# Kernel optimization log

Measured on AMD Instinct MI355X. Metric: run time of the kernel, lower is better.

## Reference

```python
import jax, jax.numpy as jnp
import numpy as np

TEMPERATURE = 0.07
EPS = 1e-12  # F.normalize eps


def _l2norm(x):
    n = jnp.linalg.norm(x, axis=-1, keepdims=True)
    return x / jnp.maximum(n, EPS)


def setup_inputs() -> dict:
    key = jax.random.key(0)
    k1, k2 = jax.random.split(key)
    B, T, H = 16, 512, 1024
    h_source = jax.random.normal(k1, (B, T, H), dtype=jnp.float32)
    h_target = jax.random.normal(k2, (B, T, H), dtype=jnp.float32)
    src_mask = jnp.ones((B, T), dtype=bool)
    tgt_mask = jnp.ones((B, T), dtype=bool)
    return {"h_source": h_source, "h_target": h_target,
            "src_mask": src_mask, "tgt_mask": tgt_mask}


def reference(h_source, h_target, src_mask, tgt_mask):
    # Masks are all-True and B*T == max_samples, so boolean selection == reshape
    # and the random subsampling branch is never taken (deterministic path).
    H = h_source.shape[-1]
    h_s = h_source.reshape(-1, H).astype(jnp.float32)          # (N, H)
    h_t = jax.lax.stop_gradient(h_target.reshape(-1, H)).astype(jnp.float32)  # detached

    h_s_norm = _l2norm(h_s)                                     # (N, H)
    h_t_norm = _l2norm(h_t)                                     # (M, H)
    sim = h_s_norm @ h_t_norm.T                                 # (N, M) cosine sim

    pos_idx = jnp.argmax(sim, axis=1)                           # == topk_idx[:, 0]
    logits = sim / TEMPERATURE
    # cross-entropy with pos_idx labels (stable log-softmax)
    logp = jax.nn.log_softmax(logits, axis=1)
    l_contrastive = -jnp.mean(jnp.take_along_axis(logp, pos_idx[:, None], axis=1)[:, 0])

    # contextual consistency: adjacent source tokens' NN embeddings should align
    nn_embeds = h_t_norm[pos_idx]                               # (N, H)
    nn_sim = jnp.sum(nn_embeds[:-1] * nn_embeds[1:], axis=-1)   # (N-1,)
    l_contextual = 1.0 - jnp.mean(nn_sim)

    return (l_contrastive, l_contextual)
```

## Files before the change

kernel.cpp:

```cpp
#include <hip/hip_runtime.h>
#include <hip/hip_bf16.h>
#include <stdint.h>


#define HDIM 1024
#define NROW 8192
#define TEMP_INV (1.0f / 0.07f)

typedef __attribute__((ext_vector_type(4))) float float4v;
typedef __attribute__((ext_vector_type(2))) float float2v;

#define SN_OFF   ((size_t)0)
#define TN_OFF   ((size_t)8388608)
#define POS_OFF  ((size_t)16777216)
#define SUM_OFF  (POS_OFF + 32768)
#define PMX_OFF  (SUM_OFF + 32768)
#define ACC_OFF  (PMX_OFF + 65536)

static __device__ __forceinline__ void gload_lds16(const void* gptr, void* lptr) {
    __builtin_amdgcn_global_load_lds(
        (const __attribute__((address_space(1))) void*)gptr,
        (__attribute__((address_space(3))) void*)(uintptr_t)(uint32_t)(uintptr_t)lptr,
        16, 0, 0);
}

static __device__ __forceinline__ float fp8dot4(unsigned a, unsigned b) {
    float2v al = __builtin_amdgcn_cvt_pk_f32_fp8((int)a, false);
    float2v ah = __builtin_amdgcn_cvt_pk_f32_fp8((int)a, true);
    float2v bl = __builtin_amdgcn_cvt_pk_f32_fp8((int)b, false);
    float2v bh = __builtin_amdgcn_cvt_pk_f32_fp8((int)b, true);
    return al[0]*bl[0] + al[1]*bl[1] + ah[0]*bh[0] + ah[1]*bh[1];
}

__global__ __launch_bounds__(256)
void norm_kernel(const float* __restrict__ hs, const float* __restrict__ ht,
                 char* __restrict__ Sn, char* __restrict__ Tn,
                 float* __restrict__ sumexp, unsigned long long* __restrict__ pmax,
                 float* __restrict__ acc) {
    const int b = blockIdx.x;
    const int t = threadIdx.x;
    const int r = t >> 4, c = t & 15;
    const float* in;
    char* outg;
    if (b < 512) { in = hs + (size_t)(b * 16 + r) * HDIM;        outg = Sn + (size_t)b * 16384; }
    else         { in = ht + (size_t)((b - 512) * 16 + r) * HDIM; outg = Tn + (size_t)(b - 512) * 16384; }

    float4v v[16];
    float ss = 0.f;
    #pragma unroll
    for (int i = 0; i < 16; ++i) {
        v[i] = ((const float4v*)in)[c * 16 + i];
        ss += v[i][0]*v[i][0] + v[i][1]*v[i][1] + v[i][2]*v[i][2] + v[i][3]*v[i][3];
    }
    #pragma unroll
    for (int off = 1; off < 16; off <<= 1) ss += __shfl_xor(ss, off);
    const float sc = 1.0f / fmaxf(sqrtf(ss), 1e-12f);

    #pragma unroll
    for (int h = 0; h < 2; ++h) {
        #pragma unroll
        for (int q = 0; q < 4; ++q) {
            const int vi = h * 8 + q * 2;
            int d0 = __builtin_amdgcn_cvt_pk_fp8_f32(v[vi][0]*sc, v[vi][1]*sc, 0, false);
            d0     = __builtin_amdgcn_cvt_pk_fp8_f32(v[vi][2]*sc, v[vi][3]*sc, d0, true);
            int d1 = __builtin_amdgcn_cvt_pk_fp8_f32(v[vi+1][0]*sc, v[vi+1][1]*sc, 0, false);
            d1     = __builtin_amdgcn_cvt_pk_fp8_f32(v[vi+1][2]*sc, v[vi+1][3]*sc, d1, true);
            uint2 pk; pk.x = (unsigned)d0; pk.y = (unsigned)d1;
            *(uint2*)(outg + (c * 2 + h) * 512 + q * 128 + r * 8) = pk;
        }
    }

    if (b < 512 && t < 16) { sumexp[b * 16 + t] = 0.f; pmax[b * 16 + t] = 0ull; }
    if (b == 0 && t == 16) { acc[0] = 0.f; acc[1] = 0.f; }
}

__global__ __launch_bounds__(512, 4)
void flash_kernel(const char* __restrict__ Sn, const char* __restrict__ Tn,
                  float* __restrict__ sumexp, unsigned long long* __restrict__ pmax) {
    __shared__ __align__(16) char As[16384];
    __shared__ __align__(16) char Bs[8192];
    __shared__ float stSe[256];
    __shared__ unsigned long long stPk[256];
    const int t = threadIdx.x;
    const int wave = t >> 6, lane = t & 63;
    const int quad = lane >> 4, l16 = lane & 15;
    const int rbase  = (int)(blockIdx.x & 31) * 256;
    const int cbase0 = (int)(blockIdx.x >> 5) * 512;

    if (t < 256) { stSe[t] = 0.f; stPk[t] = 0ull; }

    const int wm = (wave & 3) * 64, wn = (wave >> 2) * 64;

    const char* gaBase0 = Sn + (size_t)(rbase / 16 + wave * 2 + 0) * 16384 + lane * 16;
    const char* gaBase1 = Sn + (size_t)(rbase / 16 + wave * 2 + 1) * 16384 + lane * 16;

    for (int s = 0; s < 4; ++s) {
        const int cbase = cbase0 + s * 128;
        const char* ga0 = gaBase0;
        const char* ga1 = gaBase1;
        const char* gb  = Tn + (size_t)(cbase / 16 + wave) * 16384 + lane * 16;

        float4v acc[4][4];
        #pragma unroll
        for (int i = 0; i < 4; ++i)
            #pragma unroll
            for (int j = 0; j < 4; ++j) acc[i][j] = (float4v){0.f, 0.f, 0.f, 0.f};

        for (int kb = 0; kb < 16; ++kb) {
            gload_lds16(ga0, As + (wave * 2 + 0) * 1024);
            gload_lds16(ga1, As + (wave * 2 + 1) * 1024);
            gload_lds16(gb,  Bs + wave * 1024);
            ga0 += 1024; ga1 += 1024; gb += 1024;
            __syncthreads();
            #pragma unroll
            for (int ks = 0; ks < 2; ++ks) {
                long af[4], bf[4];
                #pragma unroll
                for (int i = 0; i < 4; ++i)
                    af[i] = *(const long*)(As + ((wave & 3) * 4 + i) * 1024 + ks * 512 + lane * 8);
                #pragma unroll
                for (int j = 0; j < 4; ++j)
                    bf[j] = *(const long*)(Bs + ((wave >> 2) * 4 + j) * 1024 + ks * 512 + lane * 8);
                #pragma unroll
                for (int i = 0; i < 4; ++i)
                    #pragma unroll
                    for (int j = 0; j < 4; ++j)
                        acc[i][j] = __builtin_amdgcn_mfma_f32_16x16x32_fp8_fp8(af[i], bf[j], acc[i][j], 0, 0, 0);
            }
            __syncthreads();
        }

        float* pbSe = (float*)Bs;
        unsigned long long* pbPk = (unsigned long long*)(Bs + 1024);
        float se_v[4][4]; unsigned long long pk_v[4][4];
        #pragma unroll
        for (int i = 0; i < 4; ++i) {
            #pragma unroll
            for (int r = 0; r < 4; ++r) {
                float se = 0.f; float mx = -2.f; int mi = 0x7fffffff;
                #pragma unroll
                for (int j = 0; j < 4; ++j) {
                    float v = acc[i][j][r];
                    se += __expf(v * TEMP_INV);
                    int col = cbase + wn + j * 16 + l16;
                    if (v > mx || (v == mx && col < mi)) { mx = v; mi = col; }
                }
                #pragma unroll
                for (int off = 1; off < 16; off <<= 1) {
                    se += __shfl_xor(se, off);
                    float om = __shfl_xor(mx, off);
                    int oi = __shfl_xor(mi, off);
                    if (om > mx || (om == mx && oi < mi)) { mx = om; mi = oi; }
                }
                se_v[i][r] = se;
                pk_v[i][r] = ((unsigned long long)__float_as_uint(mx + 2.0f) << 32)
                             | (unsigned long long)(0xffffffffu - (unsigned)mi);
            }
        }
        if (wave < 4 && l16 == 0) {
            #pragma unroll
            for (int i = 0; i < 4; ++i)
                #pragma unroll
                for (int r = 0; r < 4; ++r) {
                    int rl = wm + i * 16 + quad * 4 + r;
                    pbSe[rl] = se_v[i][r]; pbPk[rl] = pk_v[i][r];
                }
        }
        __syncthreads();
        if (wave >= 4 && l16 == 0) {
            #pragma unroll
            for (int i = 0; i < 4; ++i)
                #pragma unroll
                for (int r = 0; r < 4; ++r) {
                    int rl = wm + i * 16 + quad * 4 + r;
                    float se = se_v[i][r] + pbSe[rl];
                    unsigned long long pk = pk_v[i][r];
                    unsigned long long po = pbPk[rl];
                    if (po > pk) pk = po;
                    stSe[rl] += se;
                    if (pk > stPk[rl]) stPk[rl] = pk;
                }
        }
        __syncthreads();
    }

    if (t < 256) {
        atomicAdd(&sumexp[rbase + t], stSe[t]);
        atomicMax(&pmax[rbase + t], stPk[t]);
    }
}

__global__ void rowloss_kernel(const float* __restrict__ sumexp,
                               const unsigned long long* __restrict__ pmax,
                               int* __restrict__ pos, float* __restrict__ acc) {
    int r = blockIdx.x * 256 + threadIdx.x;
    unsigned long long p = pmax[r];
    float mx = __uint_as_float((unsigned)(p >> 32)) - 2.0f;
    pos[r] = (int)(0xffffffffu - (unsigned)(p & 0xffffffffu));
    float loss = logf(sumexp[r]) - mx * TEMP_INV;
    #pragma unroll
    for (int off = 1; off < 64; off <<= 1) loss += __shfl_xor(loss, off);
    __shared__ float red[4];
    if ((threadIdx.x & 63) == 0) red[threadIdx.x >> 6] = loss;
    __syncthreads();
    if (threadIdx.x == 0) atomicAdd(acc + 0, red[0] + red[1] + red[2] + red[3]);
}

__global__ __launch_bounds__(256)
void ctx_kernel(const char* __restrict__ Tn,
                const int* __restrict__ pos, float* __restrict__ acc) {
    const int wave = threadIdx.x >> 6, lane = threadIdx.x & 63;
    const int wid = blockIdx.x * 4 + wave;
    float s = 0.f;
    for (int g = wid; g < NROW - 1; g += 1024) {
        int ia = pos[g], ib = pos[g + 1];
        #pragma unroll
        for (int h = 0; h < 2; ++h) {
            int p = lane + h * 64;
            int off = (p >> 2) * 512 + (p & 3) * 128;
            uint2 va = *(const uint2*)(Tn + (size_t)(ia >> 4) * 16384 + off + (ia & 15) * 8);
            uint2 vb = *(const uint2*)(Tn + (size_t)(ib >> 4) * 16384 + off + (ib & 15) * 8);
            s += fp8dot4(va.x, vb.x);
            s += fp8dot4(va.y, vb.y);
        }
    }
    #pragma unroll
    for (int off = 1; off < 64; off <<= 1) s += __shfl_xor(s, off);
    __shared__ float red[4];
    if (lane == 0) red[wave] = s;
    __syncthreads();
    if (threadIdx.x == 0) atomicAdd(acc + 1, red[0] + red[1] + red[2] + red[3]);
}

__global__ void fin_kernel(const float* __restrict__ acc, float* __restrict__ out) {
    out[0] = acc[0] / (float)NROW;
    out[1] = 1.0f - acc[1] / (float)(NROW - 1);
}

extern "C" void kernel_launch(void* const* d_in, const int* in_sizes, int n_in,
                              void* d_out, int out_size, void* d_ws, size_t ws_size,
                              hipStream_t stream) {
    const float* hs = (const float*)d_in[0];
    const float* ht = (const float*)d_in[1];
    char* ws = (char*)d_ws;
    char* Sn = ws + SN_OFF;
    char* Tn = ws + TN_OFF;
    int*   pos = (int*)(ws + POS_OFF);
    float* sumexp = (float*)(ws + SUM_OFF);
    unsigned long long* pmax = (unsigned long long*)(ws + PMX_OFF);
    float* acc = (float*)(ws + ACC_OFF);
    float* out = (float*)d_out;

    norm_kernel<<<1024, 256, 0, stream>>>(hs, ht, Sn, Tn, sumexp, pmax, acc);
    flash_kernel<<<512, 512, 0, stream>>>(Sn, Tn, sumexp, pmax);
    rowloss_kernel<<<NROW / 256, 256, 0, stream>>>(sumexp, pmax, pos, acc);
    ctx_kernel<<<256, 256, 0, stream>>>(Tn, pos, acc);
    fin_kernel<<<1, 1, 0, stream>>>(acc, out);
}
```

Before: 254.9 us.

## Widen flash block to 1024 threads with 256x256 tiles and add row-major target copy

```diff
diff --git a/kernel.cpp b/kernel.cpp
--- a/kernel.cpp
+++ b/kernel.cpp
@@ -12,7 +12,8 @@
 
 #define SN_OFF   ((size_t)0)
 #define TN_OFF   ((size_t)8388608)
-#define POS_OFF  ((size_t)16777216)
+#define TR_OFF   ((size_t)16777216)
+#define POS_OFF  ((size_t)25165824)
 #define SUM_OFF  (POS_OFF + 32768)
 #define PMX_OFF  (SUM_OFF + 32768)
 #define ACC_OFF  (PMX_OFF + 65536)
@@ -34,7 +35,7 @@
 
 __global__ __launch_bounds__(256)
 void norm_kernel(const float* __restrict__ hs, const float* __restrict__ ht,
-                 char* __restrict__ Sn, char* __restrict__ Tn,
+                 char* __restrict__ Sn, char* __restrict__ Tn, char* __restrict__ Tr,
                  float* __restrict__ sumexp, unsigned long long* __restrict__ pmax,
                  float* __restrict__ acc) {
     const int b = blockIdx.x;
@@ -42,8 +43,10 @@
     const int r = t >> 4, c = t & 15;
     const float* in;
     char* outg;
+    char* outr = nullptr;
     if (b < 512) { in = hs + (size_t)(b * 16 + r) * HDIM;        outg = Sn + (size_t)b * 16384; }
-    else         { in = ht + (size_t)((b - 512) * 16 + r) * HDIM; outg = Tn + (size_t)(b - 512) * 16384; }
+    else         { in = ht + (size_t)((b - 512) * 16 + r) * HDIM; outg = Tn + (size_t)(b - 512) * 16384;
+                   outr = Tr + (size_t)((b - 512) * 16 + r) * HDIM; }
 
     float4v v[16];
     float ss = 0.f;
@@ -67,6 +70,7 @@
             d1     = __builtin_amdgcn_cvt_pk_fp8_f32(v[vi+1][2]*sc, v[vi+1][3]*sc, d1, true);
             uint2 pk; pk.x = (unsigned)d0; pk.y = (unsigned)d1;
             *(uint2*)(outg + (c * 2 + h) * 512 + q * 128 + r * 8) = pk;
+            if (outr) *(uint2*)(outr + c * 64 + h * 32 + q * 8) = pk;
         }
     }
 
@@ -74,11 +78,11 @@
     if (b == 0 && t == 16) { acc[0] = 0.f; acc[1] = 0.f; }
 }
 
-__global__ __launch_bounds__(512, 4)
+__global__ __launch_bounds__(1024, 4)
 void flash_kernel(const char* __restrict__ Sn, const char* __restrict__ Tn,
                   float* __restrict__ sumexp, unsigned long long* __restrict__ pmax) {
     __shared__ __align__(16) char As[16384];
-    __shared__ __align__(16) char Bs[8192];
+    __shared__ __align__(16) char Bs[16384];
     __shared__ float stSe[256];
     __shared__ unsigned long long stPk[256];
     const int t = threadIdx.x;
@@ -90,15 +94,12 @@
     if (t < 256) { stSe[t] = 0.f; stPk[t] = 0ull; }
 
     const int wm = (wave & 3) * 64, wn = (wave >> 2) * 64;
-
-    const char* gaBase0 = Sn + (size_t)(rbase / 16 + wave * 2 + 0) * 16384 + lane * 16;
-    const char* gaBase1 = Sn + (size_t)(rbase / 16 + wave * 2 + 1) * 16384 + lane * 16;
-
-    for (int s = 0; s < 4; ++s) {
-        const int cbase = cbase0 + s * 128;
-        const char* ga0 = gaBase0;
-        const char* ga1 = gaBase1;
-        const char* gb  = Tn + (size_t)(cbase / 16 + wave) * 16384 + lane * 16;
+    const char* gaBase = Sn + (size_t)(rbase / 16 + wave) * 16384 + lane * 16;
+
+    for (int s = 0; s < 2; ++s) {
+        const int cbase = cbase0 + s * 256;
+        const char* ga = gaBase;
+        const char* gb = Tn + (size_t)(cbase / 16 + wave) * 16384 + lane * 16;
 
         float4v acc[4][4];
         #pragma unroll
@@ -107,10 +108,9 @@
             for (int j = 0; j < 4; ++j) acc[i][j] = (float4v){0.f, 0.f, 0.f, 0.f};
 
         for (int kb = 0; kb < 16; ++kb) {
-            gload_lds16(ga0, As + (wave * 2 + 0) * 1024);
-            gload_lds16(ga1, As + (wave * 2 + 1) * 1024);
-            gload_lds16(gb,  Bs + wave * 1024);
-            ga0 += 1024; ga1 += 1024; gb += 1024;
+            gload_lds16(ga, As + wave * 1024);
+            gload_lds16(gb, Bs + wave * 1024);
+            ga += 1024; gb += 1024;
             __syncthreads();
             #pragma unroll
             for (int ks = 0; ks < 2; ++ks) {
@@ -131,7 +131,7 @@
         }
 
         float* pbSe = (float*)Bs;
-        unsigned long long* pbPk = (unsigned long long*)(Bs + 1024);
+        unsigned long long* pbPk = (unsigned long long*)(Bs + 4096);
         float se_v[4][4]; unsigned long long pk_v[4][4];
         #pragma unroll
         for (int i = 0; i < 4; ++i) {
@@ -157,29 +157,28 @@
                              | (unsigned long long)(0xffffffffu - (unsigned)mi);
             }
         }
-        if (wave < 4 && l16 == 0) {
+        if (l16 == 0) {
+            const int wc = wave >> 2;
             #pragma unroll
             for (int i = 0; i < 4; ++i)
                 #pragma unroll
                 for (int r = 0; r < 4; ++r) {
                     int rl = wm + i * 16 + quad * 4 + r;
-                    pbSe[rl] = se_v[i][r]; pbPk[rl] = pk_v[i][r];
+                    pbSe[wc * 256 + rl] = se_v[i][r];
+                    pbPk[wc * 256 + rl] = pk_v[i][r];
                 }
         }
         __syncthreads();
-        if (wave >= 4 && l16 == 0) {
-            #pragma unroll
-            for (int i = 0; i < 4; ++i)
-                #pragma unroll
-                for (int r = 0; r < 4; ++r) {
-                    int rl = wm + i * 16 + quad * 4 + r;
-                    float se = se_v[i][r] + pbSe[rl];
-                    unsigned long long pk = pk_v[i][r];
-                    unsigned long long po = pbPk[rl];
-                    if (po > pk) pk = po;
-                    stSe[rl] += se;
-                    if (pk > stPk[rl]) stPk[rl] = pk;
-                }
+        if (t < 256) {
+            float se = 0.f; unsigned long long pk = 0ull;
+            #pragma unroll
+            for (int w = 0; w < 4; ++w) {
+                se += pbSe[w * 256 + t];
+                unsigned long long po = pbPk[w * 256 + t];
+                if (po > pk) pk = po;
+            }
+            stSe[t] += se;
+            if (pk > stPk[t]) stPk[t] = pk;
         }
         __syncthreads();
     }
@@ -207,22 +206,17 @@
 }
 
 __global__ __launch_bounds__(256)
-void ctx_kernel(const char* __restrict__ Tn,
+void ctx_kernel(const char* __restrict__ Tr,
                 const int* __restrict__ pos, float* __restrict__ acc) {
     const int wave = threadIdx.x >> 6, lane = threadIdx.x & 63;
     const int wid = blockIdx.x * 4 + wave;
     float s = 0.f;
     for (int g = wid; g < NROW - 1; g += 1024) {
         int ia = pos[g], ib = pos[g + 1];
-        #pragma unroll
-        for (int h = 0; h < 2; ++h) {
-            int p = lane + h * 64;
-            int off = (p >> 2) * 512 + (p & 3) * 128;
-            uint2 va = *(const uint2*)(Tn + (size_t)(ia >> 4) * 16384 + off + (ia & 15) * 8);
-            uint2 vb = *(const uint2*)(Tn + (size_t)(ib >> 4) * 16384 + off + (ib & 15) * 8);
-            s += fp8dot4(va.x, vb.x);
-            s += fp8dot4(va.y, vb.y);
-        }
+        uint4 va = ((const uint4*)(Tr + (size_t)ia * HDIM))[lane];
+        uint4 vb = ((const uint4*)(Tr + (size_t)ib * HDIM))[lane];
+        s += fp8dot4(va.x, vb.x) + fp8dot4(va.y, vb.y)
+           + fp8dot4(va.z, vb.z) + fp8dot4(va.w, vb.w);
     }
     #pragma unroll
     for (int off = 1; off < 64; off <<= 1) s += __shfl_xor(s, off);
@@ -245,15 +239,16 @@
     char* ws = (char*)d_ws;
     char* Sn = ws + SN_OFF;
     char* Tn = ws + TN_OFF;
+    char* Tr = ws + TR_OFF;
     int*   pos = (int*)(ws + POS_OFF);
     float* sumexp = (float*)(ws + SUM_OFF);
     unsigned long long* pmax = (unsigned long long*)(ws + PMX_OFF);
     float* acc = (float*)(ws + ACC_OFF);
     float* out = (float*)d_out;
 
-    norm_kernel<<<1024, 256, 0, stream>>>(hs, ht, Sn, Tn, sumexp, pmax, acc);
-    flash_kernel<<<512, 512, 0, stream>>>(Sn, Tn, sumexp, pmax);
+    norm_kernel<<<1024, 256, 0, stream>>>(hs, ht, Sn, Tn, Tr, sumexp, pmax, acc);
+    flash_kernel<<<512, 1024, 0, stream>>>(Sn, Tn, sumexp, pmax);
     rowloss_kernel<<<NROW / 256, 256, 0, stream>>>(sumexp, pmax, pos, acc);
-    ctx_kernel<<<256, 256, 0, stream>>>(Tn, pos, acc);
+    ctx_kernel<<<256, 256, 0, stream>>>(Tr, pos, acc);
     fin_kernel<<<1, 1, 0, stream>>>(acc, out);
 }
```

After: 270.4 us. +6.0%, slower.

## Fuse tail kernels and add row-major FP8 target copy with coalesced norm loads

Applied to the files above, without the earlier changes.

```diff
diff --git a/kernel.cpp b/kernel.cpp
--- a/kernel.cpp
+++ b/kernel.cpp
@@ -12,10 +12,11 @@
 
 #define SN_OFF   ((size_t)0)
 #define TN_OFF   ((size_t)8388608)
-#define POS_OFF  ((size_t)16777216)
-#define SUM_OFF  (POS_OFF + 32768)
+#define TR_OFF   ((size_t)16777216)
+#define SUM_OFF  ((size_t)25165824)
 #define PMX_OFF  (SUM_OFF + 32768)
 #define ACC_OFF  (PMX_OFF + 65536)
+#define CNT_OFF  (ACC_OFF + 64)
 
 static __device__ __forceinline__ void gload_lds16(const void* gptr, void* lptr) {
     __builtin_amdgcn_global_load_lds(
@@ -34,44 +35,54 @@
 
 __global__ __launch_bounds__(256)
 void norm_kernel(const float* __restrict__ hs, const float* __restrict__ ht,
-                 char* __restrict__ Sn, char* __restrict__ Tn,
+                 char* __restrict__ Sn, char* __restrict__ Tn, char* __restrict__ Tr,
                  float* __restrict__ sumexp, unsigned long long* __restrict__ pmax,
-                 float* __restrict__ acc) {
+                 float* __restrict__ acc, unsigned* __restrict__ cnt) {
     const int b = blockIdx.x;
     const int t = threadIdx.x;
-    const int r = t >> 4, c = t & 15;
-    const float* in;
-    char* outg;
-    if (b < 512) { in = hs + (size_t)(b * 16 + r) * HDIM;        outg = Sn + (size_t)b * 16384; }
-    else         { in = ht + (size_t)((b - 512) * 16 + r) * HDIM; outg = Tn + (size_t)(b - 512) * 16384; }
+    const int wave = t >> 6, lane = t & 63;
+    const bool isT = (b >= 512);
+    const int g = isT ? (b - 512) : b;
+    const float* in = (isT ? ht : hs) + (size_t)g * 16 * HDIM;
+    char* outTiled = (isT ? Tn : Sn) + (size_t)g * 16384;
+
+    __shared__ float sq[16][256];
+    __shared__ float sscale[16];
 
     float4v v[16];
-    float ss = 0.f;
     #pragma unroll
     for (int i = 0; i < 16; ++i) {
-        v[i] = ((const float4v*)in)[c * 16 + i];
-        ss += v[i][0]*v[i][0] + v[i][1]*v[i][1] + v[i][2]*v[i][2] + v[i][3]*v[i][3];
-    }
-    #pragma unroll
-    for (int off = 1; off < 16; off <<= 1) ss += __shfl_xor(ss, off);
-    const float sc = 1.0f / fmaxf(sqrtf(ss), 1e-12f);
-
-    #pragma unroll
-    for (int h = 0; h < 2; ++h) {
-        #pragma unroll
-        for (int q = 0; q < 4; ++q) {
-            const int vi = h * 8 + q * 2;
-            int d0 = __builtin_amdgcn_cvt_pk_fp8_f32(v[vi][0]*sc, v[vi][1]*sc, 0, false);
-            d0     = __builtin_amdgcn_cvt_pk_fp8_f32(v[vi][2]*sc, v[vi][3]*sc, d0, true);
-            int d1 = __builtin_amdgcn_cvt_pk_fp8_f32(v[vi+1][0]*sc, v[vi+1][1]*sc, 0, false);
-            d1     = __builtin_amdgcn_cvt_pk_fp8_f32(v[vi+1][2]*sc, v[vi+1][3]*sc, d1, true);
-            uint2 pk; pk.x = (unsigned)d0; pk.y = (unsigned)d1;
-            *(uint2*)(outg + (c * 2 + h) * 512 + q * 128 + r * 8) = pk;
-        }
-    }
-
-    if (b < 512 && t < 16) { sumexp[b * 16 + t] = 0.f; pmax[b * 16 + t] = 0ull; }
-    if (b == 0 && t == 16) { acc[0] = 0.f; acc[1] = 0.f; }
+        v[i] = ((const float4v*)in)[i * 256 + t];
+        sq[i][t] = v[i][0]*v[i][0] + v[i][1]*v[i][1] + v[i][2]*v[i][2] + v[i][3]*v[i][3];
+    }
+    __syncthreads();
+    #pragma unroll
+    for (int j = 0; j < 4; ++j) {
+        const int ri = wave * 4 + j;
+        float s = sq[ri][lane] + sq[ri][lane + 64] + sq[ri][lane + 128] + sq[ri][lane + 192];
+        #pragma unroll
+        for (int off = 1; off < 64; off <<= 1) s += __shfl_xor(s, off);
+        if (lane == 0) sscale[ri] = 1.0f / fmaxf(sqrtf(s), 1e-12f);
+    }
+    __syncthreads();
+
+    char* tiled = (char*)sq;
+    const int koff = (t >> 3) * 512 + ((t >> 1) & 3) * 128 + (t & 1) * 4;
+    #pragma unroll
+    for (int i = 0; i < 16; ++i) {
+        const float sc = sscale[i];
+        int d = __builtin_amdgcn_cvt_pk_fp8_f32(v[i][0]*sc, v[i][1]*sc, 0, false);
+        d     = __builtin_amdgcn_cvt_pk_fp8_f32(v[i][2]*sc, v[i][3]*sc, d, true);
+        *(int*)(tiled + koff + i * 8) = d;
+        if (isT) ((int*)(Tr + (size_t)(g * 16 + i) * HDIM))[t] = d;
+    }
+    __syncthreads();
+    #pragma unroll
+    for (int j = 0; j < 4; ++j)
+        ((uint4*)outTiled)[j * 256 + t] = ((const uint4*)tiled)[j * 256 + t];
+
+    if (!isT && t < 16) { sumexp[b * 16 + t] = 0.f; pmax[b * 16 + t] = 0ull; }
+    if (b == 0 && t == 16) { acc[0] = 0.f; acc[1] = 0.f; *cnt = 0u; }
 }
 
 __global__ __launch_bounds__(512, 4)
@@ -90,7 +101,6 @@
     if (t < 256) { stSe[t] = 0.f; stPk[t] = 0ull; }
 
     const int wm = (wave & 3) * 64, wn = (wave >> 2) * 64;
-
     const char* gaBase0 = Sn + (size_t)(rbase / 16 + wave * 2 + 0) * 16384 + lane * 16;
     const char* gaBase1 = Sn + (size_t)(rbase / 16 + wave * 2 + 1) * 16384 + lane * 16;
 
@@ -190,38 +200,37 @@
     }
 }
 
-__global__ void rowloss_kernel(const float* __restrict__ sumexp,
-                               const unsigned long long* __restrict__ pmax,
-                               int* __restrict__ pos, float* __restrict__ acc) {
-    int r = blockIdx.x * 256 + threadIdx.x;
-    unsigned long long p = pmax[r];
-    float mx = __uint_as_float((unsigned)(p >> 32)) - 2.0f;
-    pos[r] = (int)(0xffffffffu - (unsigned)(p & 0xffffffffu));
-    float loss = logf(sumexp[r]) - mx * TEMP_INV;
-    #pragma unroll
-    for (int off = 1; off < 64; off <<= 1) loss += __shfl_xor(loss, off);
-    __shared__ float red[4];
-    if ((threadIdx.x & 63) == 0) red[threadIdx.x >> 6] = loss;
-    __syncthreads();
-    if (threadIdx.x == 0) atomicAdd(acc + 0, red[0] + red[1] + red[2] + red[3]);
-}
-
 __global__ __launch_bounds__(256)
-void ctx_kernel(const char* __restrict__ Tn,
-                const int* __restrict__ pos, float* __restrict__ acc) {
-    const int wave = threadIdx.x >> 6, lane = threadIdx.x & 63;
-    const int wid = blockIdx.x * 4 + wave;
+void tail_kernel(const float* __restrict__ sumexp,
+                 const unsigned long long* __restrict__ pmax,
+                 const char* __restrict__ Tr,
+                 float* __restrict__ acc, unsigned* __restrict__ cnt,
+                 float* __restrict__ out) {
+    const int blk = blockIdx.x;
+    const int t = threadIdx.x, wave = t >> 6, lane = t & 63;
+
+    if (wave == 0) {
+        int r = blk * 32 + (lane & 31);
+        unsigned long long p = pmax[r];
+        float mx = __uint_as_float((unsigned)(p >> 32)) - 2.0f;
+        float loss = logf(sumexp[r]) - mx * TEMP_INV;
+        #pragma unroll
+        for (int off = 1; off < 32; off <<= 1) loss += __shfl_xor(loss, off);
+        if (lane == 0) atomicAdd(acc + 0, loss);
+    }
+
     float s = 0.f;
-    for (int g = wid; g < NROW - 1; g += 1024) {
-        int ia = pos[g], ib = pos[g + 1];
-        #pragma unroll
-        for (int h = 0; h < 2; ++h) {
-            int p = lane + h * 64;
-            int off = (p >> 2) * 512 + (p & 3) * 128;
-            uint2 va = *(const uint2*)(Tn + (size_t)(ia >> 4) * 16384 + off + (ia & 15) * 8);
-            uint2 vb = *(const uint2*)(Tn + (size_t)(ib >> 4) * 16384 + off + (ib & 15) * 8);
-            s += fp8dot4(va.x, vb.x);
-            s += fp8dot4(va.y, vb.y);
+    #pragma unroll
+    for (int it = 0; it < 8; ++it) {
+        int g = blk * 32 + wave * 8 + it;
+        if (g < NROW - 1) {
+            unsigned long long pa = pmax[g], pb = pmax[g + 1];
+            int ia = (int)(0xffffffffu - (unsigned)(pa & 0xffffffffu));
+            int ib = (int)(0xffffffffu - (unsigned)(pb & 0xffffffffu));
+            uint4 va = ((const uint4*)(Tr + (size_t)ia * HDIM))[lane];
+            uint4 vb = ((const uint4*)(Tr + (size_t)ib * HDIM))[lane];
+            s += fp8dot4(va.x, vb.x) + fp8dot4(va.y, vb.y)
+               + fp8dot4(va.z, vb.z) + fp8dot4(va.w, vb.w);
         }
     }
     #pragma unroll
@@ -229,12 +238,18 @@
     __shared__ float red[4];
     if (lane == 0) red[wave] = s;
     __syncthreads();
-    if (threadIdx.x == 0) atomicAdd(acc + 1, red[0] + red[1] + red[2] + red[3]);
-}
-
-__global__ void fin_kernel(const float* __restrict__ acc, float* __restrict__ out) {
-    out[0] = acc[0] / (float)NROW;
-    out[1] = 1.0f - acc[1] / (float)(NROW - 1);
+    if (t == 0) atomicAdd(acc + 1, red[0] + red[1] + red[2] + red[3]);
+
+    __threadfence();
+    __shared__ unsigned done;
+    if (t == 0) done = atomicAdd(cnt, 1u);
+    __syncthreads();
+    if (t == 0 && done == 255u) {
+        float l0 = atomicAdd(acc + 0, 0.0f);
+        float l1 = atomicAdd(acc + 1, 0.0f);
+        out[0] = l0 / (float)NROW;
+        out[1] = 1.0f - l1 / (float)(NROW - 1);
+    }
 }
 
 extern "C" void kernel_launch(void* const* d_in, const int* in_sizes, int n_in,
@@ -245,15 +260,14 @@
     char* ws = (char*)d_ws;
     char* Sn = ws + SN_OFF;
     char* Tn = ws + TN_OFF;
-    int*   pos = (int*)(ws + POS_OFF);
+    char* Tr = ws + TR_OFF;
     float* sumexp = (float*)(ws + SUM_OFF);
     unsigned long long* pmax = (unsigned long long*)(ws + PMX_OFF);
     float* acc = (float*)(ws + ACC_OFF);
+    unsigned* cnt = (unsigned*)(ws + CNT_OFF);
     float* out = (float*)d_out;
 
-    norm_kernel<<<1024, 256, 0, stream>>>(hs, ht, Sn, Tn, sumexp, pmax, acc);
+    norm_kernel<<<1024, 256, 0, stream>>>(hs, ht, Sn, Tn, Tr, sumexp, pmax, acc, cnt);
     flash_kernel<<<512, 512, 0, stream>>>(Sn, Tn, sumexp, pmax);
-    rowloss_kernel<<<NROW / 256, 256, 0, stream>>>(sumexp, pmax, pos, acc);
-    ctx_kernel<<<256, 256, 0, stream>>>(Tn, pos, acc);
-    fin_kernel<<<1, 1, 0, stream>>>(acc, out);
-}
+    tail_kernel<<<256, 256, 0, stream>>>(sumexp, pmax, Tr, acc, cnt, out);
+}
```

Result: slower. 263.0 us (+3.1%).
